# Kernel tuning notes

Hardware: AMD Instinct MI355X
Metric: run time of the kernel (lower is better)

Reference implementation:

```python
import jax, jax.numpy as jnp
import numpy as np

T = 2048        # tokens
HID = 4096      # hidden_size
H = 32          # num attention heads
KV = 8          # num key/value heads (GQA)
D = HID // H    # head_dim = 128
THETA = 10000.0


def setup_inputs() -> dict:
    key = jax.random.key(0)
    k1, k2, k3 = jax.random.split(key, 3)
    hidden_states = jax.random.normal(k1, (T, HID), jnp.float32)
    positions = jnp.arange(T, dtype=jnp.int32)
    Wqkv = jax.random.normal(k2, ((H + 2 * KV) * D, HID), jnp.float32) * 0.02
    Wo = jax.random.normal(k3, (HID, H * D), jnp.float32) * 0.02
    return {"hidden_states": hidden_states, "positions": positions,
            "Wqkv": Wqkv, "Wo": Wo}


def _rope(positions, x):
    """Neox-style rotary embedding. x: [T, h, D], positions: [T]."""
    half = D // 2
    inv_freq = 1.0 / (THETA ** (jnp.arange(half, dtype=jnp.float32) / half))
    ang = positions.astype(jnp.float32)[:, None] * inv_freq      # [T, half]
    cos = jnp.cos(ang)[:, None, :]                                # [T, 1, half]
    sin = jnp.sin(ang)[:, None, :]
    x1, x2 = x[..., :half], x[..., half:]
    return jnp.concatenate([x1 * cos - x2 * sin, x2 * cos + x1 * sin], axis=-1)


def reference(hidden_states, positions, Wqkv, Wo):
    # fused QKV projection (no bias)
    qkv = hidden_states @ Wqkv.T                                  # [T, (H+2KV)*D]
    q, k, v = jnp.split(qkv, [H * D, H * D + KV * D], axis=1)
    q = q.reshape(T, H, D)
    k = k.reshape(T, KV, D)
    v = v.reshape(T, KV, D)
    # RoPE on q and k
    q = _rope(positions, q)
    k = _rope(positions, k)
    # GQA: expand kv heads to match q heads
    g = H // KV
    k = jnp.repeat(k, g, axis=1)                                  # [T, H, D]
    v = jnp.repeat(v, g, axis=1)
    # causal attention (flash-attention math)
    scores = jnp.einsum('thd,shd->hts', q, k) * (D ** -0.5)       # [H, T, T]
    causal = jnp.tril(jnp.ones((T, T), dtype=bool))
    scores = jnp.where(causal[None], scores, jnp.float32(-1e30))
    probs = jax.nn.softmax(scores, axis=-1)
    attn = jnp.einsum('hts,shd->thd', probs, v).reshape(T, H * D)
    # output projection
    return attn @ Wo.T
```

## Files before the change

### kernel.cpp

```cpp
#include <hip/hip_runtime.h>
#include <stdint.h>

#define T_SEQ 2048
#define HIDDEN 4096
#define NHEAD 32
#define NKV 8
#define HDIM 128
#define QKVN 6144

typedef __bf16 bf16x8 __attribute__((ext_vector_type(8)));
typedef float f32x4 __attribute__((ext_vector_type(4)));
typedef unsigned short u16;
typedef u16 u16x8 __attribute__((ext_vector_type(8)));
typedef u16 u16x4 __attribute__((ext_vector_type(4)));

__device__ __forceinline__ u16 f2bf(float f) {
  uint32_t u = __builtin_bit_cast(uint32_t, f);
  u = (u + 0x7fffu + ((u >> 16) & 1u)) >> 16;
  return (u16)u;
}
__device__ __forceinline__ float bf2f(u16 h) {
  uint32_t u = ((uint32_t)h) << 16;
  return __builtin_bit_cast(float, u);
}

__device__ __forceinline__ void gload16(const void* g, void* l) {
  __builtin_amdgcn_global_load_lds(
      (__attribute__((address_space(1))) void*)(uintptr_t)g,
      (__attribute__((address_space(3))) void*)(uintptr_t)l, 16, 0, 0);
}

__global__ void cvt_f32_bf16(const float* __restrict__ in, u16* __restrict__ out, int n) {
  int i = (blockIdx.x * blockDim.x + threadIdx.x) * 4;
  int stride = gridDim.x * blockDim.x * 4;
  for (; i < n; i += stride) {
    float4 v = *(const float4*)(in + i);
    u16x4 o;
    o.x = f2bf(v.x); o.y = f2bf(v.y); o.z = f2bf(v.z); o.w = f2bf(v.w);
    *(u16x4*)(out + i) = o;
  }
}

__global__ void rope_kernel(u16* __restrict__ qkv, const int* __restrict__ pos) {
  int idx = blockIdx.x * blockDim.x + threadIdx.x;
  if (idx >= T_SEQ * 40 * 64) return;
  int i = idx & 63;
  int head = (idx >> 6) % 40;
  int t = idx / (40 * 64);
  int base = head < NHEAD ? head * HDIM : NHEAD * HDIM + (head - NHEAD) * HDIM;
  float p = (float)pos[t];
  float inv_freq = exp2f(-(float)i * (13.287712379549449f / 64.0f));
  float ang = p * inv_freq;
  float s, c;
  sincosf(ang, &s, &c);
  u16* p1 = qkv + (size_t)t * QKVN + base + i;
  u16* p2 = p1 + 64;
  float x1 = bf2f(*p1), x2 = bf2f(*p2);
  *p1 = f2bf(x1 * c - x2 * s);
  *p2 = f2bf(x2 * c + x1 * s);
}

__global__ void vt_kernel(const u16* __restrict__ qkv, u16* __restrict__ vt) {
  __shared__ u16 tile[64][64];
  const int tid = threadIdx.x;
  const int tb = blockIdx.x;
  const int kvh = blockIdx.y >> 1;
  const int d0 = (blockIdx.y & 1) * 64;
  const u16* src = qkv + (size_t)(NHEAD + NKV) * HDIM + kvh * HDIM + d0;
#pragma unroll
  for (int g = 0; g < 2; ++g) {
    int u = g * 256 + tid;
    int t = u >> 3, ds = u & 7;
    u16x8 v = *(const u16x8*)(src + (size_t)(tb * 64 + t) * QKVN + ds * 8);
#pragma unroll
    for (int j = 0; j < 8; ++j) {
      int d = ds * 8 + j;
      tile[d][(((t >> 3) ^ (d & 7)) * 8) + (t & 7)] = v[j];
    }
  }
  __syncthreads();
  u16* dst = vt + ((size_t)kvh * HDIM + d0) * T_SEQ + tb * 64;
#pragma unroll
  for (int g = 0; g < 4; ++g) {
    int u = g * 256 + tid;
    int d = u >> 4, qd = u & 15;
    int a = qd >> 3, gg = (qd >> 1) & 3, b = qd & 1;
    int t0 = 32 * a + 16 * b + 4 * gg;
    u16x4 v = *(const u16x4*)&tile[d][(((t0 >> 3) ^ (d & 7)) * 8) + (t0 & 7)];
    *(u16x4*)(dst + (size_t)d * T_SEQ + qd * 4) = v;
  }
}

__device__ __forceinline__ void storeC(float* p, float v) { *p = v; }
__device__ __forceinline__ void storeC(u16* p, float v) { *p = f2bf(v); }
__device__ __forceinline__ f32x4 mfma16(bf16x8 a, bf16x8 b, f32x4 c) {
  return __builtin_amdgcn_mfma_f32_16x16x32_bf16(a, b, c, 0, 0, 0);
}

template <typename OutT, bool FUSED>
__global__ void __launch_bounds__(512, 2)
gemm256(const u16* __restrict__ A, const u16* __restrict__ B,
        OutT* __restrict__ C0, OutT* __restrict__ C1,
        int N, int K, int NT, int sliceBlocks, int nGemm,
        int nbx, int rw, int rh,
        const float* __restrict__ cvt_in, u16* __restrict__ cvt_out, int cvt_n4) {
  if (FUSED && (int)blockIdx.x >= nGemm) {
    int i = (blockIdx.x - nGemm) * blockDim.x + threadIdx.x;
    int stride = (gridDim.x - nGemm) * blockDim.x;
    for (; i < cvt_n4; i += stride) {
      float4 v = ((const float4*)cvt_in)[i];
      u16x4 o;
      o.x = f2bf(v.x); o.y = f2bf(v.y); o.z = f2bf(v.z); o.w = f2bf(v.w);
      ((u16x4*)cvt_out)[i] = o;
    }
    return;
  }

  __shared__ u16 As_[2][256 * 64];
  __shared__ u16 Bs_[2][256 * 64];

  const int tid = threadIdx.x;
  const int lane = tid & 63;
  const int w = tid >> 6;
  const int wr = w >> 2, wc = w & 3;
  const int l15 = lane & 15, lg = lane >> 4;

  const int bid = blockIdx.x;
  const int slice = bid / sliceBlocks;
  const int wi = bid % sliceBlocks;
  const int k0 = slice * (NT << 6);
  OutT* __restrict__ C = slice ? C1 : C0;

  const int c8 = wi & 7, i8 = wi >> 3;
  const int rpr = nbx / rw;
  const int by = (c8 / rpr) * rh + (i8 % rh);
  const int bx = (c8 % rpr) * rw + (i8 / rh);
  const int bm = by * 256, bn = bx * 256;

  const int u_lo = w * 64 + lane, u_hi = u_lo + 512;
  const int r0 = u_lo >> 3, s0 = (u_lo & 7) ^ (r0 & 7);
  const int r1 = u_hi >> 3, s1 = (u_hi & 7) ^ (r1 & 7);
  const u16* a0s0 = A + (size_t)(bm + r0) * K + k0 + s0 * 8;
  const u16* a0s1 = A + (size_t)(bm + r1) * K + k0 + s1 * 8;
  const u16* a1s0 = A + (size_t)(bm + 128 + r0) * K + k0 + s0 * 8;
  const u16* a1s1 = A + (size_t)(bm + 128 + r1) * K + k0 + s1 * 8;
  const u16* b0s0 = B + (size_t)(bn + r0) * K + k0 + s0 * 8;
  const u16* b0s1 = B + (size_t)(bn + r1) * K + k0 + s1 * 8;
  const u16* b1s0 = B + (size_t)(bn + 128 + r0) * K + k0 + s0 * 8;
  const u16* b1s1 = B + (size_t)(bn + 128 + r1) * K + k0 + s1 * 8;

  const int ax = l15 & 7;
  const int sl0 = (lg ^ ax) * 8;
  const int sl1 = ((4 + lg) ^ ax) * 8;
  const int a_row = (wr * 128 + l15) * 64;
  const int b_row = (wc * 64 + l15) * 64;

  f32x4 acc[8][4] = {};
  bf16x8 bfr[4][2];

#define BARRIER() asm volatile("s_barrier" ::: "memory")
#define WAITBAR(n_) asm volatile("s_waitcnt vmcnt(" #n_ ")\n\ts_barrier" ::: "memory")
#define STAGE_HALF(p0_, p1_, dst_, t_)                                         \
  {                                                                            \
    gload16((p0_) + (size_t)(t_) * 64, (dst_) + (size_t)w * 512);              \
    gload16((p1_) + (size_t)(t_) * 64, (dst_) + 4096 + (size_t)w * 512);       \
  }

  STAGE_HALF(a0s0, a0s1, &As_[0][0], 0);
  STAGE_HALF(a1s0, a1s1, &As_[0][8192], 0);
  STAGE_HALF(b0s0, b0s1, &Bs_[0][0], 0);
  STAGE_HALF(b1s0, b1s1, &Bs_[0][8192], 0);
  STAGE_HALF(b0s0, b0s1, &Bs_[1][0], 1);
  STAGE_HALF(b1s0, b1s1, &Bs_[1][8192], 1);
  WAITBAR(4);

  for (int v = 0; v < NT; ++v) {
    const int cur = v & 1, alt = cur ^ 1;
    const u16* Ac = &As_[cur][0];
    const u16* Bc = &Bs_[cur][0];
    const bool s1ok = (v + 1) < NT, s2ok = (v + 2) < NT;

#define MFMA_QUAD(p_, A0_, A1_, A2_, A3_)                                      \
    __builtin_amdgcn_s_setprio(1);                                             \
    _Pragma("unroll") for (int ni = 0; ni < 4; ++ni) {                         \
      acc[2 * (p_)][ni] = mfma16(A0_, bfr[ni][0], acc[2 * (p_)][ni]);          \
      acc[2 * (p_)][ni] = mfma16(A1_, bfr[ni][1], acc[2 * (p_)][ni]);          \
      acc[2 * (p_) + 1][ni] = mfma16(A2_, bfr[ni][0], acc[2 * (p_) + 1][ni]);  \
      acc[2 * (p_) + 1][ni] = mfma16(A3_, bfr[ni][1], acc[2 * (p_) + 1][ni]);  \
    }                                                                          \
    __builtin_amdgcn_s_setprio(0);

    {
#pragma unroll
      for (int ni = 0; ni < 4; ++ni) {
        bfr[ni][0] = *(const bf16x8*)&Bc[b_row + ni * 1024 + sl0];
        bfr[ni][1] = *(const bf16x8*)&Bc[b_row + ni * 1024 + sl1];
      }
      bf16x8 f0 = *(const bf16x8*)&Ac[a_row + 0 * 1024 + sl0];
      bf16x8 f1 = *(const bf16x8*)&Ac[a_row + 0 * 1024 + sl1];
      bf16x8 f2 = *(const bf16x8*)&Ac[a_row + 1 * 1024 + sl0];
      bf16x8 f3 = *(const bf16x8*)&Ac[a_row + 1 * 1024 + sl1];
      if (s1ok) STAGE_HALF(a0s0, a0s1, &As_[alt][0], v + 1);
      BARRIER();
      MFMA_QUAD(0, f0, f1, f2, f3);
      BARRIER();
    }
    {
      bf16x8 f0 = *(const bf16x8*)&Ac[a_row + 2 * 1024 + sl0];
      bf16x8 f1 = *(const bf16x8*)&Ac[a_row + 2 * 1024 + sl1];
      bf16x8 f2 = *(const bf16x8*)&Ac[a_row + 3 * 1024 + sl0];
      bf16x8 f3 = *(const bf16x8*)&Ac[a_row + 3 * 1024 + sl1];
      if (s1ok) STAGE_HALF(a1s0, a1s1, &As_[alt][8192], v + 1);
      if (s2ok) STAGE_HALF(b0s0, b0s1, &Bs_[cur][0], v + 2);
      BARRIER();
      MFMA_QUAD(1, f0, f1, f2, f3);
      BARRIER();
    }
    {
      bf16x8 f0 = *(const bf16x8*)&Ac[a_row + 4 * 1024 + sl0];
      bf16x8 f1 = *(const bf16x8*)&Ac[a_row + 4 * 1024 + sl1];
      bf16x8 f2 = *(const bf16x8*)&Ac[a_row + 5 * 1024 + sl0];
      bf16x8 f3 = *(const bf16x8*)&Ac[a_row + 5 * 1024 + sl1];
      if (s2ok) STAGE_HALF(b1s0, b1s1, &Bs_[cur][8192], v + 2);
      BARRIER();
      MFMA_QUAD(2, f0, f1, f2, f3);
      BARRIER();
    }
    {
      bf16x8 f0 = *(const bf16x8*)&Ac[a_row + 6 * 1024 + sl0];
      bf16x8 f1 = *(const bf16x8*)&Ac[a_row + 6 * 1024 + sl1];
      bf16x8 f2 = *(const bf16x8*)&Ac[a_row + 7 * 1024 + sl0];
      bf16x8 f3 = *(const bf16x8*)&Ac[a_row + 7 * 1024 + sl1];
      BARRIER();
      MFMA_QUAD(3, f0, f1, f2, f3);
      if (s2ok) { WAITBAR(4); } else { WAITBAR(0); }
    }
#undef MFMA_QUAD
  }

#pragma unroll
  for (int mi = 0; mi < 8; ++mi)
#pragma unroll
    for (int ni = 0; ni < 4; ++ni)
#pragma unroll
      for (int r = 0; r < 4; ++r) {
        int row = bm + wr * 128 + mi * 16 + lg * 4 + r;
        int col = bn + wc * 64 + ni * 16 + l15;
        storeC(&C[(size_t)row * N + col], acc[mi][ni][r]);
      }
#undef STAGE_HALF
#undef WAITBAR
#undef BARRIER
}

__global__ void reduce_add(float* __restrict__ out, const float* __restrict__ part, int n4) {
  int i = blockIdx.x * blockDim.x + threadIdx.x;
  int stride = gridDim.x * blockDim.x;
  for (; i < n4; i += stride) {
    float4 a = ((const float4*)out)[i];
    float4 b = ((const float4*)part)[i];
    a.x += b.x; a.y += b.y; a.z += b.z; a.w += b.w;
    ((float4*)out)[i] = a;
  }
}

__global__ void __launch_bounds__(256, 2)
attn_kernel(const u16* __restrict__ qkv, const u16* __restrict__ vt,
            u16* __restrict__ out) {
  __shared__ u16 Ksh[2][64 * 128];
  __shared__ u16 Vsh[2][128 * 64];

  const int tid = threadIdx.x;
  const int lane = tid & 63;
  const int w = tid >> 6;
  const int l15 = lane & 15, lg = lane >> 4;

  const int bid = blockIdx.x;
  const int u8 = bid & 255, sfl = bid >> 8;
  const int kvh = u8 & 7;
  const int hg = (u8 >> 3) & 3;
  const int x = (u8 >> 5) & 7;
  const int qi = sfl ? x : (15 - x);
  const int h = kvh * 4 + hg;
  const int q0 = qi * 128;
  const int nt = 2 * qi + 2;
  const int wrow = q0 + w * 32;

  const u16* Kg = qkv + NHEAD * HDIM + kvh * HDIM;
  const u16* Vg = vt + (size_t)kvh * HDIM * T_SEQ;

  bf16x8 qa[2][4];
#pragma unroll
  for (int mi = 0; mi < 2; ++mi) {
    const u16* qrow = qkv + (size_t)(wrow + mi * 16 + l15) * QKVN + h * HDIM + lg * 8;
#pragma unroll
    for (int ks = 0; ks < 4; ++ks) qa[mi][ks] = *(const bf16x8*)(qrow + ks * 32);
  }

  f32x4 acc_o[2][8] = {};
  float m[2] = {-1e30f, -1e30f}, lsum[2] = {0.f, 0.f};

  const float scale = 0.088388347648318447f;

#define STAGE_K(kv0, p)                                                        \
  {                                                                            \
    _Pragma("unroll") for (int rnd = 0; rnd < 4; ++rnd) {                      \
      int cc = rnd * 256 + tid;                                                \
      int krow = cc >> 4, kslot = cc & 15;                                     \
      gload16(Kg + (size_t)((kv0) + krow) * QKVN + (kslot ^ (krow & 7)) * 8,   \
              &Ksh[p][(rnd * 256 + w * 64) * 8]);                              \
    }                                                                          \
  }
#define STAGE_V(kv0, p)                                                        \
  {                                                                            \
    _Pragma("unroll") for (int rnd = 0; rnd < 4; ++rnd) {                      \
      int cc = rnd * 256 + tid;                                                \
      int vrow = cc >> 3, ps = cc & 7;                                         \
      gload16(Vg + (size_t)vrow * T_SEQ + (kv0) + ((ps ^ (vrow & 7)) * 8),     \
              &Vsh[p][(rnd * 256 + w * 64) * 8]);                              \
    }                                                                          \
  }

  STAGE_K(0, 0);
  STAGE_V(0, 0);
  __syncthreads();

  for (int t = 0; t < nt; ++t) {
    const int p = t & 1;
    const int kv0 = t * 64;
    const bool more = (t + 1 < nt);
    if (more) {
      STAGE_K(kv0 + 64, p ^ 1);
      STAGE_V(kv0 + 64, p ^ 1);
    }

    if (kv0 <= wrow + 31) {
      f32x4 s[2][4] = {};
#pragma unroll
      for (int ks = 0; ks < 4; ++ks) {
#pragma unroll
        for (int n = 0; n < 4; ++n) {
          int row16 = n * 16 + l15;
          bf16x8 kf = *(const bf16x8*)&Ksh[p][row16 * 128 +
                                              (((ks * 4 + lg) ^ (row16 & 7)) * 8)];
          s[0][n] = mfma16(kf, qa[0][ks], s[0][n]);
          s[1][n] = mfma16(kf, qa[1][ks], s[1][n]);
        }
      }

      const bool diag = (kv0 + 63 > wrow);
      float mx[2];
#pragma unroll
      for (int mi = 0; mi < 2; ++mi) {
        float mm = -1e30f;
        int tq = wrow + mi * 16 + l15;
#pragma unroll
        for (int n = 0; n < 4; ++n)
#pragma unroll
          for (int r = 0; r < 4; ++r) {
            float v = s[mi][n][r] * scale;
            if (diag && (kv0 + n * 16 + lg * 4 + r) > tq) v = -1e30f;
            s[mi][n][r] = v;
            mm = fmaxf(mm, v);
          }
        mm = fmaxf(mm, __shfl_xor(mm, 16, 64));
        mm = fmaxf(mm, __shfl_xor(mm, 32, 64));
        mx[mi] = mm;
      }

      float alpha[2];
#pragma unroll
      for (int mi = 0; mi < 2; ++mi) {
        float mn = fmaxf(m[mi], mx[mi]);
        alpha[mi] = __expf(m[mi] - mn);
        m[mi] = mn;
        lsum[mi] *= alpha[mi];
      }
#pragma unroll
      for (int mi = 0; mi < 2; ++mi)
#pragma unroll
        for (int r = 0; r < 4; ++r) {
          float al = __shfl(alpha[mi], lg * 4 + r, 64);
#pragma unroll
          for (int nd = 0; nd < 8; ++nd) acc_o[mi][nd][r] *= al;
        }

      bf16x8 paf[2][2];
#pragma unroll
      for (int mi = 0; mi < 2; ++mi) {
        float ps = 0.f;
#pragma unroll
        for (int n = 0; n < 4; ++n)
#pragma unroll
          for (int r = 0; r < 4; ++r) {
            float pv = __expf(s[mi][n][r] - m[mi]);
            s[mi][n][r] = pv;
            ps += pv;
          }
        ps += __shfl_xor(ps, 16, 64);
        ps += __shfl_xor(ps, 32, 64);
        lsum[mi] += ps;
#pragma unroll
        for (int ks = 0; ks < 2; ++ks) {
          u16x8 pk;
#pragma unroll
          for (int hn = 0; hn < 2; ++hn)
#pragma unroll
            for (int r = 0; r < 4; ++r)
              pk[hn * 4 + r] = f2bf(s[mi][2 * ks + hn][r]);
          paf[mi][ks] = __builtin_bit_cast(bf16x8, pk);
        }
      }

#pragma unroll
      for (int ks = 0; ks < 2; ++ks) {
#pragma unroll
        for (int nd = 0; nd < 8; ++nd) {
          int d = nd * 16 + l15;
          bf16x8 bv = *(const bf16x8*)&Vsh[p][d * 64 + (((ks * 4 + lg) ^ (d & 7)) * 8)];
          acc_o[0][nd] = mfma16(paf[0][ks], bv, acc_o[0][nd]);
          acc_o[1][nd] = mfma16(paf[1][ks], bv, acc_o[1][nd]);
        }
      }
    }

    __syncthreads();
  }

#pragma unroll
  for (int mi = 0; mi < 2; ++mi)
#pragma unroll
    for (int r = 0; r < 4; ++r) {
      float ls = __shfl(lsum[mi], lg * 4 + r, 64);
      float inv = 1.f / ls;
      int row = wrow + mi * 16 + lg * 4 + r;
#pragma unroll
      for (int nd = 0; nd < 8; ++nd) {
        int col = h * HDIM + nd * 16 + l15;
        out[(size_t)row * (NHEAD * HDIM) + col] = f2bf(acc_o[mi][nd][r] * inv);
      }
    }
#undef STAGE_K
#undef STAGE_V
}

extern "C" void kernel_launch(void* const* d_in, const int* in_sizes, int n_in,
                              void* d_out, int out_size, void* d_ws, size_t ws_size,
                              hipStream_t stream) {
  const float* hs   = (const float*)d_in[0];
  const int*   pos  = (const int*)d_in[1];
  const float* wqkv = (const float*)d_in[2];
  const float* wo   = (const float*)d_in[3];
  float* out = (float*)d_out;
  uint8_t* ws = (uint8_t*)d_ws;

  if (ws_size < 142606336u) return;
  u16* hs_bf   = (u16*)(ws + 0);
  u16* wqkv_bf = (u16*)(ws + 16777216u);
  u16* wo_bf   = (u16*)(ws + 67108864u);
  u16* qkv_bf  = (u16*)(ws + 100663296u);
  u16* attn_bf = (u16*)(ws + 125829120u);
  float* part  = (float*)(ws + 16777216u);
  u16* vt_buf  = (u16*)(ws + 0);

  cvt_f32_bf16<<<2048, 256, 0, stream>>>(hs, hs_bf, T_SEQ * HIDDEN);
  cvt_f32_bf16<<<2048, 256, 0, stream>>>(wqkv, wqkv_bf, QKVN * HIDDEN);

  gemm256<u16, true><<<256, 512, 0, stream>>>(
      hs_bf, wqkv_bf, qkv_bf, qkv_bf, QKVN, HIDDEN, 64,
      192, 192, 24, 3, 8, wo, wo_bf, (HIDDEN * HIDDEN) / 4);

  rope_kernel<<<(T_SEQ * 40 * 64) / 256, 256, 0, stream>>>(qkv_bf, pos);

  vt_kernel<<<dim3(32, 16), 256, 0, stream>>>(qkv_bf, vt_buf);

  attn_kernel<<<512, 256, 0, stream>>>(qkv_bf, vt_buf, attn_bf);

  gemm256<float, false><<<256, 512, 0, stream>>>(
      attn_bf, wo_bf, out, part, HIDDEN, HIDDEN, 32,
      128, 256, 16, 2, 8, nullptr, nullptr, 0);

  reduce_add<<<2048, 256, 0, stream>>>(out, part, (T_SEQ * HIDDEN) / 4);
}
```

Measured before the change: 321.1 us.

## Add dedicated 128x384-tile QKV GEMM and move Wo conversion into attention launch

Replaces the QKV projection, previously run through the generic 256x256 GEMM plus extra blocks converting Wo to bf16, with a dedicated kernel using 128x384 tiles. It launches 256 blocks, one per tile, so every block does GEMM work with a 3-stage B prefetch interleaved across the MFMA phases. The Wo fp32-to-bf16 conversion moves into 64 extra blocks appended to the attention kernel launch, so it overlaps with attention rather than with the QKV GEMM. The cost is lower occupancy (launch bounds of one block per CU, larger LDS use), and the attention kernel's tail blocks now compete for bandwidth.

New measurement: 386.7 us. +20.5%, slower.

```diff
diff --git a/kernel.cpp b/kernel.cpp
--- a/kernel.cpp
+++ b/kernel.cpp
@@ -97,25 +97,141 @@
   return __builtin_amdgcn_mfma_f32_16x16x32_bf16(a, b, c, 0, 0, 0);
 }
 
-template <typename OutT, bool FUSED>
+__global__ void __launch_bounds__(512, 1)
+gemm_qkv(const u16* __restrict__ A, const u16* __restrict__ B,
+         u16* __restrict__ C, int M, int N, int K) {
+  __shared__ u16 As_[2][128 * 64];
+  __shared__ u16 Bs_[2][384 * 64];
+
+  const int tid = threadIdx.x;
+  const int lane = tid & 63;
+  const int w = tid >> 6;
+  const int wr = w >> 2, wc = w & 3;
+  const int l15 = lane & 15, lg = lane >> 4;
+
+  const int c8 = blockIdx.x & 7, i8 = blockIdx.x >> 3;
+  const int by = i8 & 15;
+  const int bx = c8 * 2 + (i8 >> 4);
+  const int bm = by * 128, bn = bx * 384;
+
+  const int u_lo = w * 64 + lane, u_hi = u_lo + 512;
+  const int r0 = u_lo >> 3, s0 = (u_lo & 7) ^ (r0 & 7);
+  const int r1 = u_hi >> 3, s1 = (u_hi & 7) ^ (r1 & 7);
+  const u16* a_s0 = A + (size_t)(bm + r0) * K + s0 * 8;
+  const u16* a_s1 = A + (size_t)(bm + r1) * K + s1 * 8;
+  const u16* b_s0[3];
+  const u16* b_s1[3];
+#pragma unroll
+  for (int h = 0; h < 3; ++h) {
+    b_s0[h] = B + (size_t)(bn + h * 128 + r0) * K + s0 * 8;
+    b_s1[h] = B + (size_t)(bn + h * 128 + r1) * K + s1 * 8;
+  }
+
+  const int ax = l15 & 7;
+  const int sl0 = (lg ^ ax) * 8;
+  const int sl1 = ((4 + lg) ^ ax) * 8;
+  const int a_row = (wr * 64 + l15) * 64;
+  const int b_row = (wc * 96 + l15) * 64;
+
+  f32x4 acc[4][6] = {};
+  bf16x8 bfr[6][2];
+
+#define BARRIER() asm volatile("s_barrier" ::: "memory")
+#define WAITBAR(n_) asm volatile("s_waitcnt vmcnt(" #n_ ")\n\ts_barrier" ::: "memory")
+#define STAGE_A(t_, p_)                                                        \
+  {                                                                            \
+    gload16(a_s0 + (size_t)(t_) * 64, &As_[p_][w * 512]);                      \
+    gload16(a_s1 + (size_t)(t_) * 64, &As_[p_][4096 + w * 512]);               \
+  }
+#define STAGE_B(t_, p_, h_)                                                    \
+  {                                                                            \
+    gload16(b_s0[h_] + (size_t)(t_) * 64, &Bs_[p_][(h_) * 8192 + w * 512]);    \
+    gload16(b_s1[h_] + (size_t)(t_) * 64,                                      \
+            &Bs_[p_][(h_) * 8192 + 4096 + w * 512]);                           \
+  }
+
+  STAGE_A(0, 0);
+  STAGE_B(0, 0, 0); STAGE_B(0, 0, 1); STAGE_B(0, 0, 2);
+  STAGE_B(1, 1, 0); STAGE_B(1, 1, 1); STAGE_B(1, 1, 2);
+  WAITBAR(6);
+
+  const int NT = K >> 6;
+  for (int v = 0; v < NT; ++v) {
+    const int cur = v & 1, alt = cur ^ 1;
+    const u16* Ac = &As_[cur][0];
+    const u16* Bc = &Bs_[cur][0];
+    const bool s1ok = (v + 1) < NT, s2ok = (v + 2) < NT;
+
+#define MFMA_PH(mi_, A0_, A1_)                                                 \
+    __builtin_amdgcn_s_setprio(1);                                             \
+    _Pragma("unroll") for (int ni = 0; ni < 6; ++ni) {                         \
+      acc[mi_][ni] = mfma16(A0_, bfr[ni][0], acc[mi_][ni]);                    \
+      acc[mi_][ni] = mfma16(A1_, bfr[ni][1], acc[mi_][ni]);                    \
+    }                                                                          \
+    __builtin_amdgcn_s_setprio(0);
+
+    {
+      if (s1ok) STAGE_A(v + 1, alt);
+#pragma unroll
+      for (int ni = 0; ni < 6; ++ni) {
+        bfr[ni][0] = *(const bf16x8*)&Bc[b_row + ni * 1024 + sl0];
+        bfr[ni][1] = *(const bf16x8*)&Bc[b_row + ni * 1024 + sl1];
+      }
+      bf16x8 a0 = *(const bf16x8*)&Ac[a_row + 0 * 1024 + sl0];
+      bf16x8 a1 = *(const bf16x8*)&Ac[a_row + 0 * 1024 + sl1];
+      BARRIER();
+      MFMA_PH(0, a0, a1);
+      BARRIER();
+    }
+    {
+      if (s2ok) STAGE_B(v + 2, cur, 0);
+      bf16x8 a0 = *(const bf16x8*)&Ac[a_row + 1 * 1024 + sl0];
+      bf16x8 a1 = *(const bf16x8*)&Ac[a_row + 1 * 1024 + sl1];
+      BARRIER();
+      MFMA_PH(1, a0, a1);
+      BARRIER();
+    }
+    {
+      if (s2ok) STAGE_B(v + 2, cur, 1);
+      bf16x8 a0 = *(const bf16x8*)&Ac[a_row + 2 * 1024 + sl0];
+      bf16x8 a1 = *(const bf16x8*)&Ac[a_row + 2 * 1024 + sl1];
+      BARRIER();
+      MFMA_PH(2, a0, a1);
+      BARRIER();
+    }
+    {
+      if (s2ok) STAGE_B(v + 2, cur, 2);
+      bf16x8 a0 = *(const bf16x8*)&Ac[a_row + 3 * 1024 + sl0];
+      bf16x8 a1 = *(const bf16x8*)&Ac[a_row + 3 * 1024 + sl1];
+      BARRIER();
+      MFMA_PH(3, a0, a1);
+      if (s2ok) { WAITBAR(6); } else if (s1ok) { WAITBAR(0); } else { BARRIER(); }
+    }
+#undef MFMA_PH
+  }
+
+#pragma unroll
+  for (int mi = 0; mi < 4; ++mi)
+#pragma unroll
+    for (int ni = 0; ni < 6; ++ni)
+#pragma unroll
+      for (int r = 0; r < 4; ++r) {
+        int row = bm + wr * 64 + mi * 16 + lg * 4 + r;
+        int col = bn + wc * 96 + ni * 16 + l15;
+        storeC(&C[(size_t)row * N + col], acc[mi][ni][r]);
+      }
+#undef STAGE_A
+#undef STAGE_B
+#undef WAITBAR
+#undef BARRIER
+}
+
+template <typename OutT>
 __global__ void __launch_bounds__(512, 2)
 gemm256(const u16* __restrict__ A, const u16* __restrict__ B,
         OutT* __restrict__ C0, OutT* __restrict__ C1,
-        int N, int K, int NT, int sliceBlocks, int nGemm,
-        int nbx, int rw, int rh,
-        const float* __restrict__ cvt_in, u16* __restrict__ cvt_out, int cvt_n4) {
-  if (FUSED && (int)blockIdx.x >= nGemm) {
-    int i = (blockIdx.x - nGemm) * blockDim.x + threadIdx.x;
-    int stride = (gridDim.x - nGemm) * blockDim.x;
-    for (; i < cvt_n4; i += stride) {
-      float4 v = ((const float4*)cvt_in)[i];
-      u16x4 o;
-      o.x = f2bf(v.x); o.y = f2bf(v.y); o.z = f2bf(v.z); o.w = f2bf(v.w);
-      ((u16x4*)cvt_out)[i] = o;
-    }
-    return;
-  }
-
+        int N, int K, int NT, int sliceBlocks,
+        int nbx, int rw, int rh) {
   __shared__ u16 As_[2][256 * 64];
   __shared__ u16 Bs_[2][256 * 64];
 
@@ -266,7 +382,21 @@
 
 __global__ void __launch_bounds__(256, 2)
 attn_kernel(const u16* __restrict__ qkv, const u16* __restrict__ vt,
-            u16* __restrict__ out) {
+            u16* __restrict__ out,
+            const float* __restrict__ cvt_in, u16* __restrict__ cvt_out,
+            int cvt_n4) {
+  if ((int)blockIdx.x >= 512) {
+    int i = (blockIdx.x - 512) * blockDim.x + threadIdx.x;
+    int stride = 64 * blockDim.x;
+    for (; i < cvt_n4; i += stride) {
+      float4 v = ((const float4*)cvt_in)[i];
+      u16x4 o;
+      o.x = f2bf(v.x); o.y = f2bf(v.y); o.z = f2bf(v.z); o.w = f2bf(v.w);
+      ((u16x4*)cvt_out)[i] = o;
+    }
+    return;
+  }
+
   __shared__ u16 Ksh[2][64 * 128];
   __shared__ u16 Vsh[2][128 * 64];
 
@@ -466,19 +596,17 @@
   cvt_f32_bf16<<<2048, 256, 0, stream>>>(hs, hs_bf, T_SEQ * HIDDEN);
   cvt_f32_bf16<<<2048, 256, 0, stream>>>(wqkv, wqkv_bf, QKVN * HIDDEN);
 
-  gemm256<u16, true><<<256, 512, 0, stream>>>(
-      hs_bf, wqkv_bf, qkv_bf, qkv_bf, QKVN, HIDDEN, 64,
-      192, 192, 24, 3, 8, wo, wo_bf, (HIDDEN * HIDDEN) / 4);
+  gemm_qkv<<<256, 512, 0, stream>>>(hs_bf, wqkv_bf, qkv_bf, T_SEQ, QKVN, HIDDEN);
 
   rope_kernel<<<(T_SEQ * 40 * 64) / 256, 256, 0, stream>>>(qkv_bf, pos);
 
   vt_kernel<<<dim3(32, 16), 256, 0, stream>>>(qkv_bf, vt_buf);
 
-  attn_kernel<<<512, 256, 0, stream>>>(qkv_bf, vt_buf, attn_bf);
-
-  gemm256<float, false><<<256, 512, 0, stream>>>(
-      attn_bf, wo_bf, out, part, HIDDEN, HIDDEN, 32,
-      128, 256, 16, 2, 8, nullptr, nullptr, 0);
+  attn_kernel<<<576, 256, 0, stream>>>(qkv_bf, vt_buf, attn_bf,
+                                       wo, wo_bf, (HIDDEN * HIDDEN) / 4);
+
+  gemm256<float><<<256, 512, 0, stream>>>(
+      attn_bf, wo_bf, out, part, HIDDEN, HIDDEN, 32, 128, 16, 2, 8);
 
   reduce_add<<<2048, 256, 0, stream>>>(out, part, (T_SEQ * HIDDEN) / 4);
 }
```
